# Optimization experiments

Hardware: AMD Instinct MI355X
Metric: run time of the kernel (lower is better)

## Reference

```python
import jax, jax.numpy as jnp
import numpy as np

B, N, H, IN, D, ET = 16, 128, 256, 4, 2, 2
E = N * (N - 1)
NRF = 4 * D + 1            # num_relative_features = 9 (2D)
NODE_F = IN + NRF + D      # 15
EDGE_F = 2 * NRF + IN + D  # 24
EPS = 1e-8


def _norm(v):
    return jnp.sqrt(jnp.sum(v * v, axis=-1, keepdims=True) + EPS)


def _rot(R, v):
    return jnp.einsum('...ij,...j->...i', R, v)


def _relfeat(dp, dv, R, dth):
    # rotation-invariant relative features in frame R: rotated rel pos/vel,
    # distances, polar angles, heading difference -> 2+2+1+1+1+1+1 = 9 dims
    rp = _rot(R, dp)
    rv = _rot(R, dv)
    ang = jnp.arctan2(rp[..., 1:2], rp[..., 0:1])
    vang = jnp.arctan2(rv[..., 1:2], rv[..., 0:1])
    return jnp.concatenate([rp, rv, _norm(dp), ang, _norm(dv), vang, dth], -1)


def _forward(inputs, hidden, edges, predicted_field,
             msg_fc1_w, msg_fc1_b, msg_fc2_w, msg_fc2_b,
             pm_fc1_w, pm_fc1_b, pm_fc2_w, pm_fc2_b,
             hidden_r_w, hidden_i_w, hidden_h_w,
             present_r_w, present_r_b, present_i_w, present_i_b,
             present_n_w, present_n_b,
             input_r_w, input_r_b, input_i_w, input_i_b, input_n_w, input_n_b,
             out_w1, out_b1, out_w2, out_b2, out_w3, out_b3,
             send, recv):
    # ---- recurrent message passing on hidden state ----
    pre_msg = jnp.concatenate([hidden[:, recv], hidden[:, send]], -1)  # [B,E,2H]
    all_msgs = jnp.zeros((B, E, H), pre_msg.dtype)
    for i in range(1, ET):  # skip_first_edge_type = True
        m = jnp.tanh(pre_msg @ msg_fc1_w[i].T + msg_fc1_b[i])
        m = jnp.tanh(m @ msg_fc2_w[i].T + msg_fc2_b[i])
        all_msgs = all_msgs + m * edges[:, :, i:i + 1]
    agg_msgs = jnp.zeros((B, N, H), all_msgs.dtype).at[:, recv].add(all_msgs) / (N - 1)

    # ---- localizer: per-node frame from velocity heading ----
    ext = jnp.concatenate([inputs, predicted_field], -1)  # [B,N,6]
    pos, vel, field = ext[..., :D], ext[..., D:2 * D], ext[..., 2 * D:]
    theta = jnp.arctan2(vel[..., 1], vel[..., 0])  # [B,N]
    c, s = jnp.cos(theta), jnp.sin(theta)
    R = jnp.stack([jnp.stack([c, s], -1), jnp.stack([-s, c], -1)], -2)  # [B,N,2,2]
    Rinv = jnp.swapaxes(R, -1, -2)

    loc_pos, loc_vel, loc_field = _rot(R, pos), _rot(R, vel), _rot(R, field)
    rel_self = _relfeat(pos, vel, R, theta[..., None])
    rel_feat = jnp.concatenate([rel_self, loc_pos, loc_vel, loc_field], -1)  # [B,N,15]

    dp = pos[:, send] - pos[:, recv]
    dv = vel[:, send] - vel[:, recv]
    dth = (theta[:, send] - theta[:, recv])[..., None]
    f1 = _relfeat(dp, dv, R[:, recv], dth)
    f2 = _relfeat(-dp, -dv, R[:, send], -dth)
    edge_attr = jnp.concatenate(
        [f1, f2, loc_pos[:, recv], loc_vel[:, recv], loc_field[:, recv]], -1)  # [B,E,24]

    # ---- present (observation) message passing ----
    present_msgs = jnp.zeros((B, E, H), edge_attr.dtype)
    for i in range(1, ET):
        m = jax.nn.relu(edge_attr @ pm_fc1_w[i].T + pm_fc1_b[i])
        m = jax.nn.relu(m @ pm_fc2_w[i].T + pm_fc2_b[i])
        present_msgs = present_msgs + m * edges[:, :, i:i + 1]
    present_agg = jnp.zeros((B, N, H), present_msgs.dtype).at[:, recv].add(present_msgs) / (N - 1)

    # ---- GRU-style gated update ----
    inp_r = rel_feat @ input_r_w.T + input_r_b + present_agg @ present_r_w.T + present_r_b
    inp_i = rel_feat @ input_i_w.T + input_i_b + present_agg @ present_i_w.T + present_i_b
    inp_n = rel_feat @ input_n_w.T + input_n_b + present_agg @ present_n_w.T + present_n_b
    r = jax.nn.sigmoid(inp_r + agg_msgs @ hidden_r_w.T)
    i_g = jax.nn.sigmoid(inp_i + agg_msgs @ hidden_i_w.T)
    n_g = jnp.tanh(inp_n + r * (agg_msgs @ hidden_h_w.T))
    hidden_new = (1.0 - i_g) * n_g + i_g * hidden

    # ---- output MLP + globalizer ----
    h1 = jax.nn.relu(hidden_new @ out_w1.T + out_b1)
    h2 = jax.nn.relu(h1 @ out_w2.T + out_b2)
    pred = h2 @ out_w3.T + out_b3  # [B,N,4]
    pred_global = jnp.concatenate(
        [_rot(Rinv, pred[..., :D]), _rot(Rinv, pred[..., D:2 * D])], -1)
    outputs = inputs + pred_global
    return outputs, hidden_new


def setup_inputs():
    key = jax.random.key(0)
    ks = iter(jax.random.split(key, 48))
    rn = lambda *s: jax.random.normal(next(ks), s, jnp.float32)
    w = lambda *s: rn(*s) * 0.05
    send, recv = np.where(~np.eye(N, dtype=bool))
    return dict(
        inputs=rn(B, N, IN), hidden=rn(B, N, H),
        edges=jax.random.uniform(next(ks), (B, E, ET), jnp.float32),
        predicted_field=rn(B, N, D),
        msg_fc1_w=w(ET, H, 2 * H), msg_fc1_b=w(ET, H),
        msg_fc2_w=w(ET, H, H), msg_fc2_b=w(ET, H),
        pm_fc1_w=w(ET, H, EDGE_F), pm_fc1_b=w(ET, H),
        pm_fc2_w=w(ET, H, H), pm_fc2_b=w(ET, H),
        hidden_r_w=w(H, H), hidden_i_w=w(H, H), hidden_h_w=w(H, H),
        present_r_w=w(H, H), present_r_b=w(H),
        present_i_w=w(H, H), present_i_b=w(H),
        present_n_w=w(H, H), present_n_b=w(H),
        input_r_w=w(H, NODE_F), input_r_b=w(H),
        input_i_w=w(H, NODE_F), input_i_b=w(H),
        input_n_w=w(H, NODE_F), input_n_b=w(H),
        out_w1=w(H, H), out_b1=w(H), out_w2=w(H, H), out_b2=w(H),
        out_w3=w(IN, H), out_b3=w(IN),
        send_edges=jnp.asarray(send, jnp.int32),
        recv_edges=jnp.asarray(recv, jnp.int32),
    )


def reference(inputs, hidden, edges, predicted_field,
              msg_fc1_w, msg_fc1_b, msg_fc2_w, msg_fc2_b,
              pm_fc1_w, pm_fc1_b, pm_fc2_w, pm_fc2_b,
              hidden_r_w, hidden_i_w, hidden_h_w,
              present_r_w, present_r_b, present_i_w, present_i_b,
              present_n_w, present_n_b,
              input_r_w, input_r_b, input_i_w, input_i_b, input_n_w, input_n_b,
              out_w1, out_b1, out_w2, out_b2, out_w3, out_b3,
              send_edges, recv_edges):
    return _forward(inputs, hidden, edges, predicted_field,
                    msg_fc1_w, msg_fc1_b, msg_fc2_w, msg_fc2_b,
                    pm_fc1_w, pm_fc1_b, pm_fc2_w, pm_fc2_b,
                    hidden_r_w, hidden_i_w, hidden_h_w,
                    present_r_w, present_r_b, present_i_w, present_i_b,
                    present_n_w, present_n_b,
                    input_r_w, input_r_b, input_i_w, input_i_b, input_n_w, input_n_b,
                    out_w1, out_b1, out_w2, out_b2, out_w3, out_b3,
                    send_edges, recv_edges)
```

## Files before the change

kernel.cpp:

```cpp
#include <hip/hip_runtime.h>
#include <math.h>

#define BB 16
#define NN 128
#define HH 256
#define EE (NN*(NN-1))

typedef unsigned short ushort_t;
typedef unsigned int uint_t;
typedef __attribute__((ext_vector_type(8))) short bf16x8;
typedef __attribute__((ext_vector_type(4))) float f32x4;

__device__ __forceinline__ ushort_t f2b(float f) {
  unsigned u = __builtin_bit_cast(unsigned, f);
  unsigned r = (u + 0x7fffu + ((u >> 16) & 1u)) >> 16;
  return (ushort_t)r;
}
__device__ __forceinline__ float blo(uint_t u) {
  return __builtin_bit_cast(float, u << 16);
}
__device__ __forceinline__ float bhi(uint_t u) {
  return __builtin_bit_cast(float, u & 0xffff0000u);
}

__device__ __forceinline__ float fast_tanh(float x) {
  float xx = fminf(fmaxf(x, -15.f), 15.f);
  float e = __builtin_amdgcn_exp2f(xx * 2.8853900817779268f);
  return (e - 1.f) * __builtin_amdgcn_rcpf(e + 1.f);
}
__device__ __forceinline__ float fast_sigmoid(float x) {
  float xx = fminf(fmaxf(x, -30.f), 30.f);
  float e = __builtin_amdgcn_exp2f(-xx * 1.4426950408889634f);
  return __builtin_amdgcn_rcpf(1.f + e);
}

__global__ void k_node_geom(const float* __restrict__ inputs,
                            const float* __restrict__ pfield,
                            float* __restrict__ geom, float* __restrict__ relf) {
  int idx = blockIdx.x * blockDim.x + threadIdx.x;
  if (idx >= BB * NN) return;
  float px = inputs[idx*4+0], py = inputs[idx*4+1];
  float vx = inputs[idx*4+2], vy = inputs[idx*4+3];
  float fx = pfield[idx*2+0], fy = pfield[idx*2+1];
  float th = atan2f(vy, vx);
  float c = cosf(th), s = sinf(th);
  float lpx =  c*px + s*py, lpy = -s*px + c*py;
  float lvx =  c*vx + s*vy, lvy = -s*vx + c*vy;
  float lfx =  c*fx + s*fy, lfy = -s*fx + c*fy;
  float np_ = sqrtf(px*px + py*py + 1e-8f);
  float nv_ = sqrtf(vx*vx + vy*vy + 1e-8f);
  float ang  = atan2f(lpy, lpx);
  float vang = atan2f(lvy, lvx);
  float* g = geom + idx*16;
  g[0]=px; g[1]=py; g[2]=vx; g[3]=vy; g[4]=th; g[5]=c; g[6]=s;
  g[7]=lpx; g[8]=lpy; g[9]=lvx; g[10]=lvy; g[11]=lfx; g[12]=lfy;
  float* r = relf + idx*16;
  r[0]=lpx; r[1]=lpy; r[2]=lvx; r[3]=lvy; r[4]=np_; r[5]=ang; r[6]=nv_; r[7]=vang; r[8]=th;
  r[9]=lpx; r[10]=lpy; r[11]=lvx; r[12]=lvy; r[13]=lfx; r[14]=lfy;
}

__global__ void k_cvt(const float* __restrict__ w2, const float* __restrict__ pw2,
                      const float* __restrict__ pw1,
                      const float* __restrict__ pr_w, const float* __restrict__ pi_w,
                      const float* __restrict__ pn_w, const float* __restrict__ hr_w,
                      const float* __restrict__ hi_w, const float* __restrict__ hh_w,
                      const float* __restrict__ ow1, const float* __restrict__ ow2,
                      const float* __restrict__ w1,
                      ushort_t* __restrict__ w2b, ushort_t* __restrict__ pw2b,
                      ushort_t* __restrict__ pw1b, uint_t* __restrict__ wpk) {
  int idx = blockIdx.x * 256 + threadIdx.x;
  if (idx < HH*HH) { w2b[idx] = f2b(w2[HH*HH + idx]); return; }
  idx -= HH*HH;
  if (idx < HH*HH) { pw2b[idx] = f2b(pw2[HH*HH + idx]); return; }
  idx -= HH*HH;
  if (idx < HH*32) {
    int col = idx >> 5, kk = idx & 31;
    pw1b[idx] = (kk < 24) ? f2b(pw1[col*24 + kk]) : (ushort_t)0;
    return;
  }
  idx -= HH*32;
  if (idx >= 10*32768) return;
  int m = idx >> 15, r = idx & 32767;
  int k2 = r >> 8, h = r & 255;
  const float* src; int o0;
  if      (m == 0) { src = pr_w; o0 = h*HH + 2*k2; }
  else if (m == 1) { src = pi_w; o0 = h*HH + 2*k2; }
  else if (m == 2) { src = pn_w; o0 = h*HH + 2*k2; }
  else if (m == 3) { src = hr_w; o0 = h*HH + 2*k2; }
  else if (m == 4) { src = hi_w; o0 = h*HH + 2*k2; }
  else if (m == 5) { src = hh_w; o0 = h*HH + 2*k2; }
  else if (m == 6) { src = ow1;  o0 = h*HH + 2*k2; }
  else if (m == 7) { src = ow2;  o0 = h*HH + 2*k2; }
  else if (m == 8) { src = w1 + HH*2*HH; o0 = h*(2*HH) + 2*k2; }
  else             { src = w1 + HH*2*HH; o0 = h*(2*HH) + HH + 2*k2; }
  uint_t lo = f2b(src[o0]);
  uint_t hi = f2b(src[o0 + 1]);
  wpk[idx] = lo | (hi << 16);
}

__global__ __launch_bounds__(256) void k_hab(const float* __restrict__ hidden,
                                             const uint_t* __restrict__ wpk,
                                             const float* __restrict__ b1,
                                             float* __restrict__ Ha,
                                             float* __restrict__ Hb) {
  int n = blockIdx.x >> 2, qtr = blockIdx.x & 3;
  int tid = threadIdx.x;
  __shared__ float x[4][HH];
  for (int q = 0; q < 4; ++q) {
    int b = qtr*4 + q;
    x[q][tid] = hidden[(b*NN + n)*HH + tid];
  }
  __syncthreads();
  const uint_t* pA = wpk + 8*32768;
  const uint_t* pB = wpk + 9*32768;
  float accA[4], accB[4];
  float bias = b1[HH + tid];
  #pragma unroll
  for (int q = 0; q < 4; ++q) { accA[q] = bias; accB[q] = 0.f; }
  for (int k2 = 0; k2 < 128; ++k2) {
    uint_t ua = pA[(k2<<8) + tid];
    uint_t ub = pB[(k2<<8) + tid];
    float wa0 = blo(ua), wa1 = bhi(ua);
    float wb0 = blo(ub), wb1 = bhi(ub);
    int k = k2 << 1;
    #pragma unroll
    for (int q = 0; q < 4; ++q) {
      float2 x2 = *(const float2*)(&x[q][k]);
      accA[q] += x2.x*wa0 + x2.y*wa1;
      accB[q] += x2.x*wb0 + x2.y*wb1;
    }
  }
  for (int q = 0; q < 4; ++q) {
    int b = qtr*4 + q;
    Ha[(b*NN + n)*HH + tid] = accA[q];
    Hb[(b*NN + n)*HH + tid] = accB[q];
  }
}

__global__ __launch_bounds__(256, 4) void k_edge(
    const float* __restrict__ Ha, const float* __restrict__ Hb,
    const float* __restrict__ geom, const float* __restrict__ edges,
    const ushort_t* __restrict__ w2b, const float* __restrict__ b2,
    const ushort_t* __restrict__ pw2b, const float* __restrict__ pb2,
    const ushort_t* __restrict__ pw1b, const float* __restrict__ pb1,
    float* __restrict__ agg0, float* __restrict__ agg1,
    float* __restrict__ pagg0, float* __restrict__ pagg1) {
  int half = blockIdx.x & 1;
  int j = (blockIdx.x >> 1) & 127;
  int b = blockIdx.x >> 8;
  int tid = threadIdx.x;
  int lane = tid & 63;
  int wv = tid >> 6;
  int lrow = lane & 15, lk = lane >> 4;

  __shared__ __align__(16) unsigned char m1s[64*512];
  __shared__ __align__(16) unsigned char attrB[64*64];
  __shared__ float HajS[HH];
  __shared__ float wgtS[64];
  __shared__ float gjS[13];

  HajS[tid] = Ha[(b*NN + j)*HH + tid];
  if (tid < 13) gjS[tid] = geom[(b*NN + j)*16 + tid];
  __syncthreads();

  if (tid < 64) {
    int il = tid;
    int i = half*64 + il;
    const float* gi = geom + (b*NN + i)*16;
    float dpx = gi[0]-gjS[0], dpy = gi[1]-gjS[1];
    float dvx = gi[2]-gjS[2], dvy = gi[3]-gjS[3];
    float dth = gi[4]-gjS[4];
    float cj = gjS[5], sj = gjS[6];
    float ci = gi[5],  si = gi[6];
    float ndp = sqrtf(dpx*dpx + dpy*dpy + 1e-8f);
    float ndv = sqrtf(dvx*dvx + dvy*dvy + 1e-8f);
    float r1x =  cj*dpx + sj*dpy, r1y = -sj*dpx + cj*dpy;
    float v1x =  cj*dvx + sj*dvy, v1y = -sj*dvx + cj*dvy;
    float r2x = -(ci*dpx + si*dpy), r2y = si*dpx - ci*dpy;
    float v2x = -(ci*dvx + si*dvy), v2y = si*dvx - ci*dvy;
    float f[24];
    f[0]=r1x; f[1]=r1y; f[2]=v1x; f[3]=v1y;
    f[4]=ndp; f[5]=atan2f(r1y, r1x);
    f[6]=ndv; f[7]=atan2f(v1y, v1x); f[8]=dth;
    f[9]=r2x; f[10]=r2y; f[11]=v2x; f[12]=v2y;
    f[13]=ndp; f[14]=atan2f(r2y, r2x);
    f[15]=ndv; f[16]=atan2f(v2y, v2x); f[17]=-dth;
    f[18]=gjS[7]; f[19]=gjS[8]; f[20]=gjS[9];
    f[21]=gjS[10]; f[22]=gjS[11]; f[23]=gjS[12];
    #pragma unroll
    for (int kb = 0; kb < 4; ++kb) {
      bf16x8 v;
      #pragma unroll
      for (int e = 0; e < 8; ++e) {
        int k = kb*8 + e;
        v[e] = (k < 24) ? (short)f2b(f[k]) : (short)0;
      }
      *reinterpret_cast<bf16x8*>(attrB + il*64 + ((kb*16) ^ ((il&3)<<4))) = v;
    }
    float w = 0.f;
    if (i != j) {
      int e = i*127 + (j < i ? j : j-1);
      w = edges[(b*EE + e)*2 + 1];
    }
    wgtS[il] = w;
  }

  {
    float haj = HajS[tid];
    const float* hb = Hb + (b*NN + half*64)*HH + tid;
    #pragma unroll
    for (int i0 = 0; i0 < 64; i0 += 8) {
      float v[8];
      #pragma unroll
      for (int u = 0; u < 8; ++u) v[u] = hb[(i0+u)*HH];
      #pragma unroll
      for (int u = 0; u < 8; ++u) {
        int row = i0 + u;
        *(ushort_t*)(m1s + row*512 + ((tid*2) ^ ((row&15)<<4))) =
            f2b(fast_tanh(haj + v[u]));
      }
    }
  }
  __syncthreads();

  f32x4 zero = {0.f, 0.f, 0.f, 0.f};

  {
    f32x4 acc[4][4];
    #pragma unroll
    for (int rt = 0; rt < 4; ++rt)
      #pragma unroll
      for (int nt = 0; nt < 4; ++nt) acc[rt][nt] = zero;
    for (int kk = 0; kk < 8; ++kk) {
      bf16x8 afr[4];
      #pragma unroll
      for (int rt = 0; rt < 4; ++rt) {
        int row = rt*16 + lrow;
        afr[rt] = *reinterpret_cast<const bf16x8*>(
            m1s + row*512 + ((kk*64 + lk*16) ^ ((row&15)<<4)));
      }
      #pragma unroll
      for (int nt = 0; nt < 4; ++nt) {
        int col = wv*64 + nt*16 + lrow;
        bf16x8 bfr = *reinterpret_cast<const bf16x8*>(w2b + col*HH + kk*32 + lk*8);
        #pragma unroll
        for (int rt = 0; rt < 4; ++rt)
          acc[rt][nt] = __builtin_amdgcn_mfma_f32_16x16x32_bf16(afr[rt], bfr, acc[rt][nt], 0, 0, 0);
      }
    }
    float* aggOut = half ? agg1 : agg0;
    #pragma unroll
    for (int nt = 0; nt < 4; ++nt) {
      int col = wv*64 + nt*16 + lrow;
      float bias = b2[col];
      float p = 0.f;
      #pragma unroll
      for (int rt = 0; rt < 4; ++rt)
        #pragma unroll
        for (int r = 0; r < 4; ++r) {
          int row = rt*16 + lk*4 + r;
          p += fast_tanh(acc[rt][nt][r] + bias) * wgtS[row];
        }
      p += __shfl_xor(p, 16);
      p += __shfl_xor(p, 32);
      if (lane < 16)
        aggOut[(b*NN + j)*HH + wv*64 + nt*16 + lane] = p * (1.0f/127.0f);
    }
  }
  __syncthreads();

  {
    f32x4 acc[4][4];
    #pragma unroll
    for (int rt = 0; rt < 4; ++rt)
      #pragma unroll
      for (int nt = 0; nt < 4; ++nt) acc[rt][nt] = zero;
    bf16x8 afr[4];
    #pragma unroll
    for (int rt = 0; rt < 4; ++rt) {
      int row = rt*16 + lrow;
      afr[rt] = *reinterpret_cast<const bf16x8*>(
          attrB + row*64 + ((lk*16) ^ ((lrow&3)<<4)));
    }
    #pragma unroll
    for (int nt = 0; nt < 4; ++nt) {
      int col = wv*64 + nt*16 + lrow;
      bf16x8 bfr = *reinterpret_cast<const bf16x8*>(pw1b + col*32 + lk*8);
      #pragma unroll
      for (int rt = 0; rt < 4; ++rt)
        acc[rt][nt] = __builtin_amdgcn_mfma_f32_16x16x32_bf16(afr[rt], bfr, acc[rt][nt], 0, 0, 0);
    }
    #pragma unroll
    for (int nt = 0; nt < 4; ++nt) {
      int col = wv*64 + nt*16 + lrow;
      float bias = pb1[col];
      #pragma unroll
      for (int rt = 0; rt < 4; ++rt)
        #pragma unroll
        for (int r = 0; r < 4; ++r) {
          int row = rt*16 + lk*4 + r;
          *(ushort_t*)(m1s + row*512 + ((col*2) ^ ((row&15)<<4))) =
              f2b(fmaxf(acc[rt][nt][r] + bias, 0.f));
        }
    }
  }
  __syncthreads();

  {
    f32x4 acc[4][4];
    #pragma unroll
    for (int rt = 0; rt < 4; ++rt)
      #pragma unroll
      for (int nt = 0; nt < 4; ++nt) acc[rt][nt] = zero;
    for (int kk = 0; kk < 8; ++kk) {
      bf16x8 afr[4];
      #pragma unroll
      for (int rt = 0; rt < 4; ++rt) {
        int row = rt*16 + lrow;
        afr[rt] = *reinterpret_cast<const bf16x8*>(
            m1s + row*512 + ((kk*64 + lk*16) ^ ((row&15)<<4)));
      }
      #pragma unroll
      for (int nt = 0; nt < 4; ++nt) {
        int col = wv*64 + nt*16 + lrow;
        bf16x8 bfr = *reinterpret_cast<const bf16x8*>(pw2b + col*HH + kk*32 + lk*8);
        #pragma unroll
        for (int rt = 0; rt < 4; ++rt)
          acc[rt][nt] = __builtin_amdgcn_mfma_f32_16x16x32_bf16(afr[rt], bfr, acc[rt][nt], 0, 0, 0);
      }
    }
    float* paggOut = half ? pagg1 : pagg0;
    #pragma unroll
    for (int nt = 0; nt < 4; ++nt) {
      int col = wv*64 + nt*16 + lrow;
      float bias = pb2[col];
      float p = 0.f;
      #pragma unroll
      for (int rt = 0; rt < 4; ++rt)
        #pragma unroll
        for (int r = 0; r < 4; ++r) {
          int row = rt*16 + lk*4 + r;
          p += fmaxf(acc[rt][nt][r] + bias, 0.f) * wgtS[row];
        }
      p += __shfl_xor(p, 16);
      p += __shfl_xor(p, 32);
      if (lane < 16)
        paggOut[(b*NN + j)*HH + wv*64 + nt*16 + lane] = p * (1.0f/127.0f);
    }
  }
}

__global__ __launch_bounds__(256) void k_gru(
    const float* __restrict__ inputs, const float* __restrict__ hidden,
    const float* __restrict__ geom, const float* __restrict__ relf,
    const float* __restrict__ agg0, const float* __restrict__ agg1,
    const float* __restrict__ pagg0, const float* __restrict__ pagg1,
    const uint_t* __restrict__ wpk,
    const float* __restrict__ pr_b, const float* __restrict__ pi_b,
    const float* __restrict__ pn_b,
    const float* __restrict__ ir_w, const float* __restrict__ ir_b,
    const float* __restrict__ ii_w, const float* __restrict__ ii_b,
    const float* __restrict__ in_w, const float* __restrict__ in_b,
    const float* __restrict__ ob1, const float* __restrict__ ob2,
    const float* __restrict__ ow3, const float* __restrict__ ob3,
    float* __restrict__ out_o, float* __restrict__ out_h) {
  int n = blockIdx.x >> 2, qtr = blockIdx.x & 3;
  int tid = threadIdx.x;
  __shared__ float paS[4][HH], agS[4][HH], hS[4][HH], t0S[4][HH], t1S[4][HH];
  __shared__ float relS[4][16];
  __shared__ float predS[4][4];

  for (int q = 0; q < 4; ++q) {
    int b = qtr*4 + q;
    int base = (b*NN + n)*HH;
    paS[q][tid] = pagg0[base + tid] + pagg1[base + tid];
    agS[q][tid] = agg0[base + tid] + agg1[base + tid];
    hS[q][tid]  = hidden[base + tid];
  }
  if (tid < 64) {
    int q = tid >> 4, k = tid & 15;
    int b = qtr*4 + q;
    relS[q][k] = (k < 15) ? relf[(b*NN + n)*16 + k] : 0.f;
  }
  __syncthreads();

  int h = tid;
  const uint_t* pPr = wpk;
  const uint_t* pPi = wpk + 32768;
  const uint_t* pPn = wpk + 2*32768;
  const uint_t* pHr = wpk + 3*32768;
  const uint_t* pHi = wpk + 4*32768;
  const uint_t* pHh = wpk + 5*32768;
  const uint_t* pO1 = wpk + 6*32768;
  const uint_t* pO2 = wpk + 7*32768;

  float aR[4], aI[4], aN[4], aH[4];
  float br = ir_b[h] + pr_b[h];
  float bi = ii_b[h] + pi_b[h];
  float bn = in_b[h] + pn_b[h];
  #pragma unroll
  for (int q = 0; q < 4; ++q) { aR[q]=br; aI[q]=bi; aN[q]=bn; aH[q]=0.f; }

  for (int k = 0; k < 15; ++k) {
    float wr = ir_w[h*15+k], wi = ii_w[h*15+k], wn = in_w[h*15+k];
    #pragma unroll
    for (int q = 0; q < 4; ++q) {
      float x = relS[q][k];
      aR[q] += x*wr; aI[q] += x*wi; aN[q] += x*wn;
    }
  }

  for (int k2 = 0; k2 < 128; ++k2) {
    uint_t upr = pPr[(k2<<8) + h];
    uint_t upi = pPi[(k2<<8) + h];
    uint_t upn = pPn[(k2<<8) + h];
    uint_t uhr = pHr[(k2<<8) + h];
    uint_t uhi = pHi[(k2<<8) + h];
    uint_t uhh = pHh[(k2<<8) + h];
    float pr0 = blo(upr), pr1 = bhi(upr);
    float pi0 = blo(upi), pi1 = bhi(upi);
    float pn0 = blo(upn), pn1 = bhi(upn);
    float hr0 = blo(uhr), hr1 = bhi(uhr);
    float hi0 = blo(uhi), hi1 = bhi(uhi);
    float hh0 = blo(uhh), hh1 = bhi(uhh);
    int k = k2 << 1;
    #pragma unroll
    for (int q = 0; q < 4; ++q) {
      float2 xp = *(const float2*)(&paS[q][k]);
      float2 xa = *(const float2*)(&agS[q][k]);
      aR[q] += xp.x*pr0 + xp.y*pr1 + xa.x*hr0 + xa.y*hr1;
      aI[q] += xp.x*pi0 + xp.y*pi1 + xa.x*hi0 + xa.y*hi1;
      aN[q] += xp.x*pn0 + xp.y*pn1;
      aH[q] += xa.x*hh0 + xa.y*hh1;
    }
  }

  #pragma unroll
  for (int q = 0; q < 4; ++q) {
    int b = qtr*4 + q;
    float r  = fast_sigmoid(aR[q]);
    float ig = fast_sigmoid(aI[q]);
    float ng = fast_tanh(aN[q] + r*aH[q]);
    float hn = (1.f - ig)*ng + ig*hS[q][h];
    out_h[(b*NN + n)*HH + h] = hn;
    t0S[q][h] = hn;
  }
  __syncthreads();

  {
    float a1[4];
    float bias = ob1[h];
    #pragma unroll
    for (int q = 0; q < 4; ++q) a1[q] = bias;
    for (int k2 = 0; k2 < 128; ++k2) {
      uint_t u = pO1[(k2<<8) + h];
      float w0 = blo(u), w1 = bhi(u);
      int k = k2 << 1;
      #pragma unroll
      for (int q = 0; q < 4; ++q) {
        float2 x2 = *(const float2*)(&t0S[q][k]);
        a1[q] += x2.x*w0 + x2.y*w1;
      }
    }
    __syncthreads();
    #pragma unroll
    for (int q = 0; q < 4; ++q) t1S[q][h] = fmaxf(a1[q], 0.f);
  }
  __syncthreads();

  {
    float a2[4];
    float bias = ob2[h];
    #pragma unroll
    for (int q = 0; q < 4; ++q) a2[q] = bias;
    for (int k2 = 0; k2 < 128; ++k2) {
      uint_t u = pO2[(k2<<8) + h];
      float w0 = blo(u), w1 = bhi(u);
      int k = k2 << 1;
      #pragma unroll
      for (int q = 0; q < 4; ++q) {
        float2 x2 = *(const float2*)(&t1S[q][k]);
        a2[q] += x2.x*w0 + x2.y*w1;
      }
    }
    __syncthreads();
    #pragma unroll
    for (int q = 0; q < 4; ++q) t0S[q][h] = fmaxf(a2[q], 0.f);
  }
  __syncthreads();

  if (tid < 16) {
    int o = tid >> 2, q = tid & 3;
    float acc = ob3[o];
    for (int k = 0; k < HH; ++k) acc += t0S[q][k]*ow3[o*HH + k];
    predS[q][o] = acc;
  }
  __syncthreads();
  if (tid < 4) {
    int q = tid;
    int b = qtr*4 + q;
    const float* g = geom + (b*NN + n)*16;
    float c = g[5], s = g[6];
    float p0 = predS[q][0], p1 = predS[q][1], p2 = predS[q][2], p3 = predS[q][3];
    int base = (b*NN + n)*4;
    out_o[base+0] = inputs[base+0] + (c*p0 - s*p1);
    out_o[base+1] = inputs[base+1] + (s*p0 + c*p1);
    out_o[base+2] = inputs[base+2] + (c*p2 - s*p3);
    out_o[base+3] = inputs[base+3] + (s*p2 + c*p3);
  }
}

extern "C" void kernel_launch(void* const* d_in, const int* in_sizes, int n_in,
                              void* d_out, int out_size, void* d_ws, size_t ws_size,
                              hipStream_t stream) {
  const float* inputs    = (const float*)d_in[0];
  const float* hidden    = (const float*)d_in[1];
  const float* edges     = (const float*)d_in[2];
  const float* pfield    = (const float*)d_in[3];
  const float* msg_fc1_w = (const float*)d_in[4];
  const float* msg_fc1_b = (const float*)d_in[5];
  const float* msg_fc2_w = (const float*)d_in[6];
  const float* msg_fc2_b = (const float*)d_in[7];
  const float* pm_fc1_w  = (const float*)d_in[8];
  const float* pm_fc1_b  = (const float*)d_in[9];
  const float* pm_fc2_w  = (const float*)d_in[10];
  const float* pm_fc2_b  = (const float*)d_in[11];
  const float* hr_w = (const float*)d_in[12];
  const float* hi_w = (const float*)d_in[13];
  const float* hh_w = (const float*)d_in[14];
  const float* pr_w = (const float*)d_in[15];
  const float* pr_b = (const float*)d_in[16];
  const float* pi_w = (const float*)d_in[17];
  const float* pi_b = (const float*)d_in[18];
  const float* pn_w = (const float*)d_in[19];
  const float* pn_b = (const float*)d_in[20];
  const float* ir_w = (const float*)d_in[21];
  const float* ir_b = (const float*)d_in[22];
  const float* ii_w = (const float*)d_in[23];
  const float* ii_b = (const float*)d_in[24];
  const float* in_w = (const float*)d_in[25];
  const float* in_b = (const float*)d_in[26];
  const float* ow1  = (const float*)d_in[27];
  const float* ob1  = (const float*)d_in[28];
  const float* ow2  = (const float*)d_in[29];
  const float* ob2  = (const float*)d_in[30];
  const float* ow3  = (const float*)d_in[31];
  const float* ob3  = (const float*)d_in[32];

  float* ws   = (float*)d_ws;
  float* geom = ws;
  float* relf = geom + 32768;
  float* Ha   = relf + 32768;
  float* Hb   = Ha   + 524288;
  float* agg0 = Hb   + 524288;
  float* agg1 = agg0 + 524288;
  float* pagg0= agg1 + 524288;
  float* pagg1= pagg0+ 524288;
  ushort_t* w2b  = (ushort_t*)(pagg1 + 524288);
  ushort_t* pw2b = w2b + HH*HH;
  ushort_t* pw1b = pw2b + HH*HH;
  uint_t*   wpk  = (uint_t*)(pw1b + HH*32);

  float* out_o = (float*)d_out;
  float* out_h = out_o + BB*NN*4;

  k_node_geom<<<dim3(8), dim3(256), 0, stream>>>(inputs, pfield, geom, relf);
  k_cvt<<<dim3(1824), dim3(256), 0, stream>>>(msg_fc2_w, pm_fc2_w,
      pm_fc1_w + HH*24, pr_w, pi_w, pn_w, hr_w, hi_w, hh_w, ow1, ow2,
      msg_fc1_w, w2b, pw2b, pw1b, wpk);
  k_hab<<<dim3(512), dim3(256), 0, stream>>>(hidden, wpk, msg_fc1_b, Ha, Hb);
  k_edge<<<dim3(BB*NN*2), dim3(256), 0, stream>>>(Ha, Hb, geom, edges,
      w2b, msg_fc2_b + HH, pw2b, pm_fc2_b + HH,
      pw1b, pm_fc1_b + HH, agg0, agg1, pagg0, pagg1);
  k_gru<<<dim3(512), dim3(256), 0, stream>>>(inputs, hidden, geom, relf,
      agg0, agg1, pagg0, pagg1, wpk,
      pr_b, pi_b, pn_b, ir_w, ir_b, ii_w, ii_b, in_w, in_b,
      ob1, ob2, ow3, ob3, out_o, out_h);
}
```

Before: 393.4 us.

## Merge prep kernels, tile weight packing via LDS, vectorize tanh staging, preload biases

Merges the node-geometry and weight-conversion kernels into one launch, and rewrites the packed-weight transpose to go through a shared-memory tile so global reads and writes are coalesced. In the edge kernel, the tanh(Ha+Hb) staging now loads float2 and writes packed bf16 pairs. MFMA accumulators start from the bias instead of zero, and edge weights are cached in registers. These cut launch overhead, uncoalesced transposed accesses and per-element epilogue work, at the cost of an extra barrier and more registers.

```diff
diff --git a/kernel.cpp b/kernel.cpp
--- a/kernel.cpp
+++ b/kernel.cpp
@@ -34,68 +34,86 @@
   return __builtin_amdgcn_rcpf(1.f + e);
 }
 
-__global__ void k_node_geom(const float* __restrict__ inputs,
-                            const float* __restrict__ pfield,
-                            float* __restrict__ geom, float* __restrict__ relf) {
-  int idx = blockIdx.x * blockDim.x + threadIdx.x;
-  if (idx >= BB * NN) return;
-  float px = inputs[idx*4+0], py = inputs[idx*4+1];
-  float vx = inputs[idx*4+2], vy = inputs[idx*4+3];
-  float fx = pfield[idx*2+0], fy = pfield[idx*2+1];
-  float th = atan2f(vy, vx);
-  float c = cosf(th), s = sinf(th);
-  float lpx =  c*px + s*py, lpy = -s*px + c*py;
-  float lvx =  c*vx + s*vy, lvy = -s*vx + c*vy;
-  float lfx =  c*fx + s*fy, lfy = -s*fx + c*fy;
-  float np_ = sqrtf(px*px + py*py + 1e-8f);
-  float nv_ = sqrtf(vx*vx + vy*vy + 1e-8f);
-  float ang  = atan2f(lpy, lpx);
-  float vang = atan2f(lvy, lvx);
-  float* g = geom + idx*16;
-  g[0]=px; g[1]=py; g[2]=vx; g[3]=vy; g[4]=th; g[5]=c; g[6]=s;
-  g[7]=lpx; g[8]=lpy; g[9]=lvx; g[10]=lvy; g[11]=lfx; g[12]=lfy;
-  float* r = relf + idx*16;
-  r[0]=lpx; r[1]=lpy; r[2]=lvx; r[3]=lvy; r[4]=np_; r[5]=ang; r[6]=nv_; r[7]=vang; r[8]=th;
-  r[9]=lpx; r[10]=lpy; r[11]=lvx; r[12]=lvy; r[13]=lfx; r[14]=lfy;
-}
-
-__global__ void k_cvt(const float* __restrict__ w2, const float* __restrict__ pw2,
-                      const float* __restrict__ pw1,
-                      const float* __restrict__ pr_w, const float* __restrict__ pi_w,
-                      const float* __restrict__ pn_w, const float* __restrict__ hr_w,
-                      const float* __restrict__ hi_w, const float* __restrict__ hh_w,
-                      const float* __restrict__ ow1, const float* __restrict__ ow2,
-                      const float* __restrict__ w1,
-                      ushort_t* __restrict__ w2b, ushort_t* __restrict__ pw2b,
-                      ushort_t* __restrict__ pw1b, uint_t* __restrict__ wpk) {
-  int idx = blockIdx.x * 256 + threadIdx.x;
-  if (idx < HH*HH) { w2b[idx] = f2b(w2[HH*HH + idx]); return; }
-  idx -= HH*HH;
-  if (idx < HH*HH) { pw2b[idx] = f2b(pw2[HH*HH + idx]); return; }
-  idx -= HH*HH;
-  if (idx < HH*32) {
+__global__ __launch_bounds__(256) void k_prep(
+    const float* __restrict__ inputs, const float* __restrict__ pfield,
+    float* __restrict__ geom, float* __restrict__ relf,
+    const float* __restrict__ w2, const float* __restrict__ pw2,
+    const float* __restrict__ pw1,
+    const float* __restrict__ pr_w, const float* __restrict__ pi_w,
+    const float* __restrict__ pn_w, const float* __restrict__ hr_w,
+    const float* __restrict__ hi_w, const float* __restrict__ hh_w,
+    const float* __restrict__ ow1, const float* __restrict__ ow2,
+    const float* __restrict__ w1,
+    ushort_t* __restrict__ w2b, ushort_t* __restrict__ pw2b,
+    ushort_t* __restrict__ pw1b, uint_t* __restrict__ wpk) {
+  __shared__ float ltile[64][65];
+  int bid = blockIdx.x;
+  int tid = threadIdx.x;
+
+  if (bid < 8) {
+    int idx = bid * 256 + tid;
+    float px = inputs[idx*4+0], py = inputs[idx*4+1];
+    float vx = inputs[idx*4+2], vy = inputs[idx*4+3];
+    float fx = pfield[idx*2+0], fy = pfield[idx*2+1];
+    float th = atan2f(vy, vx);
+    float c = cosf(th), s = sinf(th);
+    float lpx =  c*px + s*py, lpy = -s*px + c*py;
+    float lvx =  c*vx + s*vy, lvy = -s*vx + c*vy;
+    float lfx =  c*fx + s*fy, lfy = -s*fx + c*fy;
+    float np_ = sqrtf(px*px + py*py + 1e-8f);
+    float nv_ = sqrtf(vx*vx + vy*vy + 1e-8f);
+    float ang  = atan2f(lpy, lpx);
+    float vang = atan2f(lvy, lvx);
+    float* g = geom + idx*16;
+    g[0]=px; g[1]=py; g[2]=vx; g[3]=vy; g[4]=th; g[5]=c; g[6]=s;
+    g[7]=lpx; g[8]=lpy; g[9]=lvx; g[10]=lvy; g[11]=lfx; g[12]=lfy;
+    float* r = relf + idx*16;
+    r[0]=lpx; r[1]=lpy; r[2]=lvx; r[3]=lvy; r[4]=np_; r[5]=ang; r[6]=nv_; r[7]=vang; r[8]=th;
+    r[9]=lpx; r[10]=lpy; r[11]=lvx; r[12]=lvy; r[13]=lfx; r[14]=lfy;
+    return;
+  }
+  if (bid < 552) {
+    int idx = (bid - 8) * 256 + tid;
+    if (idx < HH*HH) { w2b[idx] = f2b(w2[HH*HH + idx]); return; }
+    idx -= HH*HH;
+    if (idx < HH*HH) { pw2b[idx] = f2b(pw2[HH*HH + idx]); return; }
+    idx -= HH*HH;
     int col = idx >> 5, kk = idx & 31;
     pw1b[idx] = (kk < 24) ? f2b(pw1[col*24 + kk]) : (ushort_t)0;
     return;
   }
-  idx -= HH*32;
-  if (idx >= 10*32768) return;
-  int m = idx >> 15, r = idx & 32767;
-  int k2 = r >> 8, h = r & 255;
-  const float* src; int o0;
-  if      (m == 0) { src = pr_w; o0 = h*HH + 2*k2; }
-  else if (m == 1) { src = pi_w; o0 = h*HH + 2*k2; }
-  else if (m == 2) { src = pn_w; o0 = h*HH + 2*k2; }
-  else if (m == 3) { src = hr_w; o0 = h*HH + 2*k2; }
-  else if (m == 4) { src = hi_w; o0 = h*HH + 2*k2; }
-  else if (m == 5) { src = hh_w; o0 = h*HH + 2*k2; }
-  else if (m == 6) { src = ow1;  o0 = h*HH + 2*k2; }
-  else if (m == 7) { src = ow2;  o0 = h*HH + 2*k2; }
-  else if (m == 8) { src = w1 + HH*2*HH; o0 = h*(2*HH) + 2*k2; }
-  else             { src = w1 + HH*2*HH; o0 = h*(2*HH) + HH + 2*k2; }
-  uint_t lo = f2b(src[o0]);
-  uint_t hi = f2b(src[o0 + 1]);
-  wpk[idx] = lo | (hi << 16);
+  int tb = bid - 552;
+  int m  = tb >> 4;
+  int sub = tb & 15;
+  int Hbase  = (sub >> 2) * 64;
+  int k2base = (sub & 3) * 32;
+  const float* src; int sstride, soff;
+  if      (m == 0) { src = pr_w; sstride = HH; soff = 0; }
+  else if (m == 1) { src = pi_w; sstride = HH; soff = 0; }
+  else if (m == 2) { src = pn_w; sstride = HH; soff = 0; }
+  else if (m == 3) { src = hr_w; sstride = HH; soff = 0; }
+  else if (m == 4) { src = hi_w; sstride = HH; soff = 0; }
+  else if (m == 5) { src = hh_w; sstride = HH; soff = 0; }
+  else if (m == 6) { src = ow1;  sstride = HH; soff = 0; }
+  else if (m == 7) { src = ow2;  sstride = HH; soff = 0; }
+  else if (m == 8) { src = w1 + HH*2*HH; sstride = 2*HH; soff = 0; }
+  else             { src = w1 + HH*2*HH; sstride = 2*HH; soff = HH; }
+  int wv = tid >> 6, lane = tid & 63;
+  #pragma unroll 4
+  for (int i = 0; i < 16; ++i) {
+    int rl = wv*16 + i;
+    ltile[rl][lane] = src[(Hbase + rl)*sstride + soff + 2*k2base + lane];
+  }
+  __syncthreads();
+  int h_l = tid & 63, kslot = tid >> 6;
+  uint_t* dst = wpk + m*32768;
+  #pragma unroll
+  for (int e = 0; e < 8; ++e) {
+    int kk = kslot*8 + e;
+    uint_t lo = f2b(ltile[h_l][2*kk]);
+    uint_t hi = f2b(ltile[h_l][2*kk + 1]);
+    dst[(k2base + kk)*256 + Hbase + h_l] = lo | (hi << 16);
+  }
 }
 
 __global__ __launch_bounds__(256) void k_hab(const float* __restrict__ hidden,
@@ -155,7 +173,7 @@
 
   __shared__ __align__(16) unsigned char m1s[64*512];
   __shared__ __align__(16) unsigned char attrB[64*64];
-  __shared__ float HajS[HH];
+  __shared__ __align__(16) float HajS[HH];
   __shared__ float wgtS[64];
   __shared__ float gjS[13];
 
@@ -204,33 +222,52 @@
     }
     wgtS[il] = w;
   }
+  __syncthreads();
 
   {
-    float haj = HajS[tid];
-    const float* hb = Hb + (b*NN + half*64)*HH + tid;
-    #pragma unroll
-    for (int i0 = 0; i0 < 64; i0 += 8) {
-      float v[8];
-      #pragma unroll
-      for (int u = 0; u < 8; ++u) v[u] = hb[(i0+u)*HH];
+    int hp = tid & 127;
+    int rh = tid >> 7;
+    float2 ha2 = *(const float2*)(HajS + 2*hp);
+    const float* hbbase = Hb + (b*NN + half*64 + rh*32)*HH + 2*hp;
+    #pragma unroll
+    for (int r0 = 0; r0 < 32; r0 += 8) {
+      float2 v[8];
+      #pragma unroll
+      for (int u = 0; u < 8; ++u)
+        v[u] = *(const float2*)(hbbase + (r0+u)*HH);
       #pragma unroll
       for (int u = 0; u < 8; ++u) {
-        int row = i0 + u;
-        *(ushort_t*)(m1s + row*512 + ((tid*2) ^ ((row&15)<<4))) =
-            f2b(fast_tanh(haj + v[u]));
-      }
-    }
-  }
-  __syncthreads();
-
-  f32x4 zero = {0.f, 0.f, 0.f, 0.f};
+        int row = rh*32 + r0 + u;
+        uint_t lo = f2b(fast_tanh(ha2.x + v[u].x));
+        uint_t hi = f2b(fast_tanh(ha2.y + v[u].y));
+        *(uint_t*)(m1s + row*512 + ((hp*4) ^ ((row&15)<<4))) = lo | (hi << 16);
+      }
+    }
+  }
+  __syncthreads();
+
+  float wreg[16];
+  #pragma unroll
+  for (int rt = 0; rt < 4; ++rt)
+    #pragma unroll
+    for (int r = 0; r < 4; ++r)
+      wreg[rt*4+r] = wgtS[rt*16 + lk*4 + r];
 
   {
     f32x4 acc[4][4];
-    #pragma unroll
-    for (int rt = 0; rt < 4; ++rt)
-      #pragma unroll
-      for (int nt = 0; nt < 4; ++nt) acc[rt][nt] = zero;
+    {
+      float bias0 = b2[wv*64 + 0*16 + lrow];
+      float bias1 = b2[wv*64 + 1*16 + lrow];
+      float bias2 = b2[wv*64 + 2*16 + lrow];
+      float bias3 = b2[wv*64 + 3*16 + lrow];
+      #pragma unroll
+      for (int rt = 0; rt < 4; ++rt) {
+        acc[rt][0] = (f32x4){bias0,bias0,bias0,bias0};
+        acc[rt][1] = (f32x4){bias1,bias1,bias1,bias1};
+        acc[rt][2] = (f32x4){bias2,bias2,bias2,bias2};
+        acc[rt][3] = (f32x4){bias3,bias3,bias3,bias3};
+      }
+    }
     for (int kk = 0; kk < 8; ++kk) {
       bf16x8 afr[4];
       #pragma unroll
@@ -251,16 +288,12 @@
     float* aggOut = half ? agg1 : agg0;
     #pragma unroll
     for (int nt = 0; nt < 4; ++nt) {
-      int col = wv*64 + nt*16 + lrow;
-      float bias = b2[col];
       float p = 0.f;
       #pragma unroll
       for (int rt = 0; rt < 4; ++rt)
         #pragma unroll
-        for (int r = 0; r < 4; ++r) {
-          int row = rt*16 + lk*4 + r;
-          p += fast_tanh(acc[rt][nt][r] + bias) * wgtS[row];
-        }
+        for (int r = 0; r < 4; ++r)
+          p += fast_tanh(acc[rt][nt][r]) * wreg[rt*4+r];
       p += __shfl_xor(p, 16);
       p += __shfl_xor(p, 32);
       if (lane < 16)
@@ -271,10 +304,19 @@
 
   {
     f32x4 acc[4][4];
-    #pragma unroll
-    for (int rt = 0; rt < 4; ++rt)
-      #pragma unroll
-      for (int nt = 0; nt < 4; ++nt) acc[rt][nt] = zero;
+    {
+      float bias0 = pb1[wv*64 + 0*16 + lrow];
+      float bias1 = pb1[wv*64 + 1*16 + lrow];
+      float bias2 = pb1[wv*64 + 2*16 + lrow];
+      float bias3 = pb1[wv*64 + 3*16 + lrow];
+      #pragma unroll
+      for (int rt = 0; rt < 4; ++rt) {
+        acc[rt][0] = (f32x4){bias0,bias0,bias0,bias0};
+        acc[rt][1] = (f32x4){bias1,bias1,bias1,bias1};
+        acc[rt][2] = (f32x4){bias2,bias2,bias2,bias2};
+        acc[rt][3] = (f32x4){bias3,bias3,bias3,bias3};
+      }
+    }
     bf16x8 afr[4];
     #pragma unroll
     for (int rt = 0; rt < 4; ++rt) {
@@ -293,14 +335,13 @@
     #pragma unroll
     for (int nt = 0; nt < 4; ++nt) {
       int col = wv*64 + nt*16 + lrow;
-      float bias = pb1[col];
       #pragma unroll
       for (int rt = 0; rt < 4; ++rt)
         #pragma unroll
         for (int r = 0; r < 4; ++r) {
           int row = rt*16 + lk*4 + r;
           *(ushort_t*)(m1s + row*512 + ((col*2) ^ ((row&15)<<4))) =
-              f2b(fmaxf(acc[rt][nt][r] + bias, 0.f));
+              f2b(fmaxf(acc[rt][nt][r], 0.f));
         }
     }
   }
@@ -308,10 +349,19 @@
 
   {
     f32x4 acc[4][4];
-    #pragma unroll
-    for (int rt = 0; rt < 4; ++rt)
-      #pragma unroll
-      for (int nt = 0; nt < 4; ++nt) acc[rt][nt] = zero;
+    {
+      float bias0 = pb2[wv*64 + 0*16 + lrow];
+      float bias1 = pb2[wv*64 + 1*16 + lrow];
+      float bias2 = pb2[wv*64 + 2*16 + lrow];
+      float bias3 = pb2[wv*64 + 3*16 + lrow];
+      #pragma unroll
+      for (int rt = 0; rt < 4; ++rt) {
+        acc[rt][0] = (f32x4){bias0,bias0,bias0,bias0};
+        acc[rt][1] = (f32x4){bias1,bias1,bias1,bias1};
+        acc[rt][2] = (f32x4){bias2,bias2,bias2,bias2};
+        acc[rt][3] = (f32x4){bias3,bias3,bias3,bias3};
+      }
+    }
     for (int kk = 0; kk < 8; ++kk) {
       bf16x8 afr[4];
       #pragma unroll
@@ -332,16 +382,12 @@
     float* paggOut = half ? pagg1 : pagg0;
     #pragma unroll
     for (int nt = 0; nt < 4; ++nt) {
-      int col = wv*64 + nt*16 + lrow;
-      float bias = pb2[col];
       float p = 0.f;
       #pragma unroll
       for (int rt = 0; rt < 4; ++rt)
         #pragma unroll
-        for (int r = 0; r < 4; ++r) {
-          int row = rt*16 + lk*4 + r;
-          p += fmaxf(acc[rt][nt][r] + bias, 0.f) * wgtS[row];
-        }
+        for (int r = 0; r < 4; ++r)
+          p += fmaxf(acc[rt][nt][r], 0.f) * wreg[rt*4+r];
       p += __shfl_xor(p, 16);
       p += __shfl_xor(p, 32);
       if (lane < 16)
@@ -564,9 +610,9 @@
   float* out_o = (float*)d_out;
   float* out_h = out_o + BB*NN*4;
 
-  k_node_geom<<<dim3(8), dim3(256), 0, stream>>>(inputs, pfield, geom, relf);
-  k_cvt<<<dim3(1824), dim3(256), 0, stream>>>(msg_fc2_w, pm_fc2_w,
-      pm_fc1_w + HH*24, pr_w, pi_w, pn_w, hr_w, hi_w, hh_w, ow1, ow2,
+  k_prep<<<dim3(712), dim3(256), 0, stream>>>(inputs, pfield, geom, relf,
+      msg_fc2_w, pm_fc2_w, pm_fc1_w + HH*24,
+      pr_w, pi_w, pn_w, hr_w, hi_w, hh_w, ow1, ow2,
       msg_fc1_w, w2b, pw2b, pw1b, wpk);
   k_hab<<<dim3(512), dim3(256), 0, stream>>>(hidden, wpk, msg_fc1_b, Ha, Hb);
   k_edge<<<dim3(BB*NN*2), dim3(256), 0, stream>>>(Ha, Hb, geom, edges,
```

New measurement: 411.6 us. 4.6% more time.
